# Kernel optimization log

Measured on AMD Instinct MI355X. Metric: run time of the kernel, lower is better.

The kernel has to match this reference:

```python
import jax, jax.numpy as jnp
import numpy as np

KH, KW = 5, 5            # local window (h, w), must be odd
SIGMA = 1.0
GAUSS_DEN = 2.0 * SIGMA ** 2
N, C, H, W = 4, 20, 64, 2048


def setup_inputs() -> dict:
    key = jax.random.key(0)
    k1, k2, k3 = jax.random.split(key, 3)
    xyz = jax.random.normal(k1, (N, 3, H, W), dtype=jnp.float32)
    softmax = jax.random.uniform(k2, (N, C, H, W), dtype=jnp.float32)
    mask = jax.random.randint(k3, (N, H, W), 0, 2).astype(jnp.bool_)
    return {"xyz": xyz, "softmax": softmax, "mask": mask}


def reference(xyz, softmax, mask):
    # xyz: [N,3,H,W], softmax: [N,C,H,W], mask: [N,H,W]
    sm = softmax * mask[:, None].astype(softmax.dtype)
    ph, pw = KH // 2, KW // 2
    # zero padding matches F.unfold's implicit zero padding
    xyz_p = jnp.pad(xyz, ((0, 0), (0, 0), (ph, ph), (pw, pw)))
    sm_p = jnp.pad(sm, ((0, 0), (0, 0), (ph, ph), (pw, pw)))
    out = jnp.zeros_like(sm)
    # Fused form of the im2col math: for each window offset, weight the
    # shifted (masked) softmax by the XYZ-distance Gaussian and accumulate.
    # 25 static offsets -> small fixed unrolled loop, no giant unfold buffers.
    for dy in range(KH):
        for dx in range(KW):
            wxyz = xyz_p[:, :, dy:dy + sm.shape[2], dx:dx + sm.shape[3]]  # [N,3,H,W]
            d2 = jnp.sum((wxyz - xyz) ** 2, axis=1)                       # [N,H,W]
            g = jnp.exp(-d2 / GAUSS_DEN)                                  # [N,H,W]
            out = out + g[:, None] * sm_p[:, :, dy:dy + sm.shape[2], dx:dx + sm.shape[3]]
    return out
```

## Files before the change

### kernel.cpp

```cpp
#include <hip/hip_runtime.h>

#define NN 4
#define CC 20
#define HH 64
#define WW 2048
#define CG 4
#define CPG (CC / CG)
#define PX 4

__global__ __launch_bounds__(256, 4) void lc_xyz_kernel(
    const float* __restrict__ xyz,
    const float* __restrict__ softmax,
    const int* __restrict__ mask,
    float* __restrict__ out)
{
    const int t  = blockIdx.x * blockDim.x + threadIdx.x;
    const int h  = blockIdx.y;
    const int nz = blockIdx.z;
    const int n  = nz >> 2;
    const int cg = nz & 3;
    const int hw = HH * WW;
    const int p0 = t * PX;

    const float* xb  = xyz     + (size_t)n * 3  * hw;
    const float* smb = softmax + (size_t)n * CC * hw + (size_t)(cg * CPG) * hw;
    const int*   mb  = mask    + (size_t)n * hw;

    const int ctr = h * WW + p0;
    const float4 cxv = *(const float4*)(xb + 0 * hw + ctr);
    const float4 cyv = *(const float4*)(xb + 1 * hw + ctr);
    const float4 czv = *(const float4*)(xb + 2 * hw + ctr);
    const float cx[PX] = {cxv.x, cxv.y, cxv.z, cxv.w};
    const float cy[PX] = {cyv.x, cyv.y, cyv.z, cyv.w};
    const float cz[PX] = {czv.x, czv.y, czv.z, czv.w};

    float acc[CPG][PX];
#pragma unroll
    for (int c = 0; c < CPG; ++c)
#pragma unroll
        for (int i = 0; i < PX; ++i) acc[c][i] = 0.f;

    int c0 = p0 - 4; if (c0 < 0) c0 = 0;
    const int c1 = p0;
    int c2 = p0 + 4; if (c2 > WW - 4) c2 = WW - 4;

    float vf[12];
#pragma unroll
    for (int j = 2; j <= 9; ++j)
        vf[j] = ((unsigned)(p0 - 4 + j) < (unsigned)WW) ? 1.f : 0.f;

#pragma unroll
    for (int dy = -2; dy <= 2; ++dy) {
        const int row = h + dy;
        if ((unsigned)row >= (unsigned)HH) continue;
        const int rb = row * WW;

        const int4 m0 = *(const int4*)(mb + rb + c0);
        const int4 m1 = *(const int4*)(mb + rb + c1);
        const int4 m2 = *(const int4*)(mb + rb + c2);
        const float4 x0 = *(const float4*)(xb + 0 * hw + rb + c0);
        const float4 x1 = *(const float4*)(xb + 0 * hw + rb + c1);
        const float4 x2 = *(const float4*)(xb + 0 * hw + rb + c2);
        const float4 y0 = *(const float4*)(xb + 1 * hw + rb + c0);
        const float4 y1 = *(const float4*)(xb + 1 * hw + rb + c1);
        const float4 y2 = *(const float4*)(xb + 1 * hw + rb + c2);
        const float4 z0 = *(const float4*)(xb + 2 * hw + rb + c0);
        const float4 z1 = *(const float4*)(xb + 2 * hw + rb + c1);
        const float4 z2 = *(const float4*)(xb + 2 * hw + rb + c2);

        const float xw[12] = {x0.x,x0.y,x0.z,x0.w, x1.x,x1.y,x1.z,x1.w, x2.x,x2.y,x2.z,x2.w};
        const float yw[12] = {y0.x,y0.y,y0.z,y0.w, y1.x,y1.y,y1.z,y1.w, y2.x,y2.y,y2.z,y2.w};
        const float zw[12] = {z0.x,z0.y,z0.z,z0.w, z1.x,z1.y,z1.z,z1.w, z2.x,z2.y,z2.z,z2.w};
        const int   mi[12] = {m0.x,m0.y,m0.z,m0.w, m1.x,m1.y,m1.z,m1.w, m2.x,m2.y,m2.z,m2.w};

        float mf[12];
#pragma unroll
        for (int j = 2; j <= 9; ++j) mf[j] = vf[j] * (float)mi[j];

        float g[PX][5];
#pragma unroll
        for (int i = 0; i < PX; ++i) {
#pragma unroll
            for (int dx = 0; dx < 5; ++dx) {
                const int j = i + dx + 2;
                const float ax = xw[j] - cx[i];
                const float ay = yw[j] - cy[i];
                const float az = zw[j] - cz[i];
                const float d2 = ax * ax + ay * ay + az * az;
                g[i][dx] = mf[j] * __expf(-0.5f * d2);
            }
        }

#pragma unroll
        for (int c = 0; c < CPG; ++c) {
            const float* sp = smb + (size_t)c * hw + rb;
            const float4 s0 = *(const float4*)(sp + c0);
            const float4 s1 = *(const float4*)(sp + c1);
            const float4 s2 = *(const float4*)(sp + c2);
            const float sw[12] = {s0.x,s0.y,s0.z,s0.w, s1.x,s1.y,s1.z,s1.w, s2.x,s2.y,s2.z,s2.w};
#pragma unroll
            for (int i = 0; i < PX; ++i) {
                float a = acc[c][i];
#pragma unroll
                for (int dx = 0; dx < 5; ++dx)
                    a = fmaf(g[i][dx], sw[i + dx + 2], a);
                acc[c][i] = a;
            }
        }
    }

    float* ob = out + (size_t)n * CC * hw + (size_t)(cg * CPG) * hw + ctr;
#pragma unroll
    for (int c = 0; c < CPG; ++c)
        *(float4*)(ob + (size_t)c * hw) =
            make_float4(acc[c][0], acc[c][1], acc[c][2], acc[c][3]);
}

extern "C" void kernel_launch(void* const* d_in, const int* in_sizes, int n_in,
                              void* d_out, int out_size, void* d_ws, size_t ws_size,
                              hipStream_t stream) {
    const float* xyz     = (const float*)d_in[0];
    const float* softmax = (const float*)d_in[1];
    const int*   mask    = (const int*)d_in[2];
    float*       out     = (float*)d_out;

    dim3 block(256, 1, 1);
    dim3 grid(WW / (PX * 256), HH, NN * CG);
    hipLaunchKernelGGL(lc_xyz_kernel, grid, block, 0, stream,
                       xyz, softmax, mask, out);
}
```

Baseline: 134.0 us.

## Compute two output rows per thread and remap grid to a swizzled 1D index

Each thread now produces outputs for two adjacent rows, so the 6 loaded input rows (xyz, mask, softmax) are shared between both rows instead of reloading 5 rows per output row. This cuts the redundant global and L2 traffic of the vertical stencil. The grid is flattened to 1D with a swizzle that groups the batch/channel-group index in the low bits, presumably for better cache locality across blocks. Register pressure roughly doubles for the accumulators and the launch bound drops to 3 blocks per CU, which may lower occupancy.

```diff
diff --git a/kernel.cpp b/kernel.cpp
--- a/kernel.cpp
+++ b/kernel.cpp
@@ -7,38 +7,46 @@
 #define CG 4
 #define CPG (CC / CG)
 #define PX 4
+#define HB 2
 
-__global__ __launch_bounds__(256, 4) void lc_xyz_kernel(
+__global__ __launch_bounds__(256, 3) void lc_xyz_kernel(
     const float* __restrict__ xyz,
     const float* __restrict__ softmax,
     const int* __restrict__ mask,
     float* __restrict__ out)
 {
-    const int t  = blockIdx.x * blockDim.x + threadIdx.x;
-    const int h  = blockIdx.y;
-    const int nz = blockIdx.z;
-    const int n  = nz >> 2;
-    const int cg = nz & 3;
+    const unsigned id = blockIdx.x;
+    const int z  = (int)(id & 7u) + (int)((id >> 9) << 3);
+    const int jj = (int)((id >> 3) & 63u);
+    const int hp = jj >> 1;
+    const int xb = jj & 1;
+    const int n  = z >> 2;
+    const int cg = z & 3;
+    const int h0 = hp * HB;
+    const int t  = xb * 256 + (int)threadIdx.x;
+    const int p0 = t * PX;
     const int hw = HH * WW;
-    const int p0 = t * PX;
 
-    const float* xb  = xyz     + (size_t)n * 3  * hw;
-    const float* smb = softmax + (size_t)n * CC * hw + (size_t)(cg * CPG) * hw;
-    const int*   mb  = mask    + (size_t)n * hw;
+    const float* xbse = xyz     + (size_t)n * 3  * hw;
+    const float* smb  = softmax + (size_t)n * CC * hw + (size_t)(cg * CPG) * hw;
+    const int*   mb   = mask    + (size_t)n * hw;
 
-    const int ctr = h * WW + p0;
-    const float4 cxv = *(const float4*)(xb + 0 * hw + ctr);
-    const float4 cyv = *(const float4*)(xb + 1 * hw + ctr);
-    const float4 czv = *(const float4*)(xb + 2 * hw + ctr);
-    const float cx[PX] = {cxv.x, cxv.y, cxv.z, cxv.w};
-    const float cy[PX] = {cyv.x, cyv.y, cyv.z, cyv.w};
-    const float cz[PX] = {czv.x, czv.y, czv.z, czv.w};
+    const int ctr0 = h0 * WW + p0;
+    const float4 cxv0 = *(const float4*)(xbse + 0 * hw + ctr0);
+    const float4 cyv0 = *(const float4*)(xbse + 1 * hw + ctr0);
+    const float4 czv0 = *(const float4*)(xbse + 2 * hw + ctr0);
+    const float4 cxv1 = *(const float4*)(xbse + 0 * hw + ctr0 + WW);
+    const float4 cyv1 = *(const float4*)(xbse + 1 * hw + ctr0 + WW);
+    const float4 czv1 = *(const float4*)(xbse + 2 * hw + ctr0 + WW);
+    const float cx[2][PX] = {{cxv0.x, cxv0.y, cxv0.z, cxv0.w}, {cxv1.x, cxv1.y, cxv1.z, cxv1.w}};
+    const float cy[2][PX] = {{cyv0.x, cyv0.y, cyv0.z, cyv0.w}, {cyv1.x, cyv1.y, cyv1.z, cyv1.w}};
+    const float cz[2][PX] = {{czv0.x, czv0.y, czv0.z, czv0.w}, {czv1.x, czv1.y, czv1.z, czv1.w}};
 
-    float acc[CPG][PX];
+    float acc0[CPG][PX], acc1[CPG][PX];
 #pragma unroll
     for (int c = 0; c < CPG; ++c)
 #pragma unroll
-        for (int i = 0; i < PX; ++i) acc[c][i] = 0.f;
+        for (int i = 0; i < PX; ++i) { acc0[c][i] = 0.f; acc1[c][i] = 0.f; }
 
     int c0 = p0 - 4; if (c0 < 0) c0 = 0;
     const int c1 = p0;
@@ -46,27 +54,27 @@
 
     float vf[12];
 #pragma unroll
-    for (int j = 2; j <= 9; ++j)
-        vf[j] = ((unsigned)(p0 - 4 + j) < (unsigned)WW) ? 1.f : 0.f;
+    for (int q = 2; q <= 9; ++q)
+        vf[q] = ((unsigned)(p0 - 4 + q) < (unsigned)WW) ? 1.f : 0.f;
 
 #pragma unroll
-    for (int dy = -2; dy <= 2; ++dy) {
-        const int row = h + dy;
+    for (int dr = -2; dr <= 3; ++dr) {
+        const int row = h0 + dr;
         if ((unsigned)row >= (unsigned)HH) continue;
         const int rb = row * WW;
 
         const int4 m0 = *(const int4*)(mb + rb + c0);
         const int4 m1 = *(const int4*)(mb + rb + c1);
         const int4 m2 = *(const int4*)(mb + rb + c2);
-        const float4 x0 = *(const float4*)(xb + 0 * hw + rb + c0);
-        const float4 x1 = *(const float4*)(xb + 0 * hw + rb + c1);
-        const float4 x2 = *(const float4*)(xb + 0 * hw + rb + c2);
-        const float4 y0 = *(const float4*)(xb + 1 * hw + rb + c0);
-        const float4 y1 = *(const float4*)(xb + 1 * hw + rb + c1);
-        const float4 y2 = *(const float4*)(xb + 1 * hw + rb + c2);
-        const float4 z0 = *(const float4*)(xb + 2 * hw + rb + c0);
-        const float4 z1 = *(const float4*)(xb + 2 * hw + rb + c1);
-        const float4 z2 = *(const float4*)(xb + 2 * hw + rb + c2);
+        const float4 x0 = *(const float4*)(xbse + 0 * hw + rb + c0);
+        const float4 x1 = *(const float4*)(xbse + 0 * hw + rb + c1);
+        const float4 x2 = *(const float4*)(xbse + 0 * hw + rb + c2);
+        const float4 y0 = *(const float4*)(xbse + 1 * hw + rb + c0);
+        const float4 y1 = *(const float4*)(xbse + 1 * hw + rb + c1);
+        const float4 y2 = *(const float4*)(xbse + 1 * hw + rb + c2);
+        const float4 z0 = *(const float4*)(xbse + 2 * hw + rb + c0);
+        const float4 z1 = *(const float4*)(xbse + 2 * hw + rb + c1);
+        const float4 z2 = *(const float4*)(xbse + 2 * hw + rb + c2);
 
         const float xw[12] = {x0.x,x0.y,x0.z,x0.w, x1.x,x1.y,x1.z,x1.w, x2.x,x2.y,x2.z,x2.w};
         const float yw[12] = {y0.x,y0.y,y0.z,y0.w, y1.x,y1.y,y1.z,y1.w, y2.x,y2.y,y2.z,y2.w};
@@ -75,20 +83,37 @@
 
         float mf[12];
 #pragma unroll
-        for (int j = 2; j <= 9; ++j) mf[j] = vf[j] * (float)mi[j];
+        for (int q = 2; q <= 9; ++q) mf[q] = vf[q] * (float)mi[q];
 
-        float g[PX][5];
+        const bool act0 = (dr <= 2);
+        const bool act1 = (dr >= -1);
+
+        float g0[PX][5], g1[PX][5];
+        if (act0) {
 #pragma unroll
-        for (int i = 0; i < PX; ++i) {
+            for (int i = 0; i < PX; ++i)
 #pragma unroll
-            for (int dx = 0; dx < 5; ++dx) {
-                const int j = i + dx + 2;
-                const float ax = xw[j] - cx[i];
-                const float ay = yw[j] - cy[i];
-                const float az = zw[j] - cz[i];
-                const float d2 = ax * ax + ay * ay + az * az;
-                g[i][dx] = mf[j] * __expf(-0.5f * d2);
-            }
+                for (int dx = 0; dx < 5; ++dx) {
+                    const int q = i + dx + 2;
+                    const float ax = xw[q] - cx[0][i];
+                    const float ay = yw[q] - cy[0][i];
+                    const float az = zw[q] - cz[0][i];
+                    const float d2 = ax * ax + ay * ay + az * az;
+                    g0[i][dx] = mf[q] * __expf(-0.5f * d2);
+                }
+        }
+        if (act1) {
+#pragma unroll
+            for (int i = 0; i < PX; ++i)
+#pragma unroll
+                for (int dx = 0; dx < 5; ++dx) {
+                    const int q = i + dx + 2;
+                    const float ax = xw[q] - cx[1][i];
+                    const float ay = yw[q] - cy[1][i];
+                    const float az = zw[q] - cz[1][i];
+                    const float d2 = ax * ax + ay * ay + az * az;
+                    g1[i][dx] = mf[q] * __expf(-0.5f * d2);
+                }
         }
 
 #pragma unroll
@@ -98,22 +123,37 @@
             const float4 s1 = *(const float4*)(sp + c1);
             const float4 s2 = *(const float4*)(sp + c2);
             const float sw[12] = {s0.x,s0.y,s0.z,s0.w, s1.x,s1.y,s1.z,s1.w, s2.x,s2.y,s2.z,s2.w};
+            if (act0) {
 #pragma unroll
-            for (int i = 0; i < PX; ++i) {
-                float a = acc[c][i];
+                for (int i = 0; i < PX; ++i) {
+                    float a = acc0[c][i];
 #pragma unroll
-                for (int dx = 0; dx < 5; ++dx)
-                    a = fmaf(g[i][dx], sw[i + dx + 2], a);
-                acc[c][i] = a;
+                    for (int dx = 0; dx < 5; ++dx)
+                        a = fmaf(g0[i][dx], sw[i + dx + 2], a);
+                    acc0[c][i] = a;
+                }
+            }
+            if (act1) {
+#pragma unroll
+                for (int i = 0; i < PX; ++i) {
+                    float a = acc1[c][i];
+#pragma unroll
+                    for (int dx = 0; dx < 5; ++dx)
+                        a = fmaf(g1[i][dx], sw[i + dx + 2], a);
+                    acc1[c][i] = a;
+                }
             }
         }
     }
 
-    float* ob = out + (size_t)n * CC * hw + (size_t)(cg * CPG) * hw + ctr;
+    float* ob = out + (size_t)n * CC * hw + (size_t)(cg * CPG) * hw + ctr0;
 #pragma unroll
-    for (int c = 0; c < CPG; ++c)
+    for (int c = 0; c < CPG; ++c) {
         *(float4*)(ob + (size_t)c * hw) =
-            make_float4(acc[c][0], acc[c][1], acc[c][2], acc[c][3]);
+            make_float4(acc0[c][0], acc0[c][1], acc0[c][2], acc0[c][3]);
+        *(float4*)(ob + (size_t)c * hw + WW) =
+            make_float4(acc1[c][0], acc1[c][1], acc1[c][2], acc1[c][3]);
+    }
 }
 
 extern "C" void kernel_launch(void* const* d_in, const int* in_sizes, int n_in,
@@ -125,7 +165,7 @@
     float*       out     = (float*)d_out;
 
     dim3 block(256, 1, 1);
-    dim3 grid(WW / (PX * 256), HH, NN * CG);
+    dim3 grid((WW / (PX * 256)) * (HH / HB) * (NN * CG), 1, 1);
     hipLaunchKernelGGL(lc_xyz_kernel, grid, block, 0, stream,
                        xyz, softmax, mask, out);
 }
```

Result: slower. 201.1 us (+50.1%).
